# Kernel optimization log

Measured on AMD Instinct MI355X. Metric: run time of the kernel, lower is better.

The kernel has to match this reference:

```python
import jax, jax.numpy as jnp
import numpy as np

B, N, E, D, AD = 8, 1000, 4, 64, 32  # batch, n_node, n_edge_types, state_dim, annotation_dim
W_SCALE = 0.02  # matches normal_(0.0, 0.02) init


def setup_inputs() -> dict:
    key = jax.random.key(0)
    ks = jax.random.split(key, 10)
    return {
        "prop_state": jax.random.normal(ks[0], (B, N, D), jnp.float32),
        "annotation": jax.random.normal(ks[1], (B, N, AD), jnp.float32),
        "A": jax.random.uniform(ks[2], (B, N, 2 * N * E), jnp.float32),
        "W_in": W_SCALE * jax.random.normal(ks[3], (E, D, D), jnp.float32),
        "W_out": W_SCALE * jax.random.normal(ks[4], (E, D, D), jnp.float32),
        "W_r": W_SCALE * jax.random.normal(ks[5], (D, 3 * D), jnp.float32),
        "W_z": W_SCALE * jax.random.normal(ks[6], (D, 3 * D), jnp.float32),
        "W_h": W_SCALE * jax.random.normal(ks[7], (D, 3 * D), jnp.float32),
        "Wo1": W_SCALE * jax.random.normal(ks[8], (D, D + AD), jnp.float32),
        "Wo2": W_SCALE * jax.random.normal(ks[9], (1, D), jnp.float32),
    }


def _propagate(state, A_in, A_out, W_in, W_out, W_r, W_z, W_h):
    b, n, d = state.shape
    e = W_in.shape[0]
    # per-edge-type linear transforms (torch Linear: y = x @ W.T), batched over edge types
    # layout matches torch: stack over e then transpose(0,1) -> [b, e, n, d] -> [b, e*n, d]
    s_in = jnp.einsum('bnd,efd->benf', state, W_in).reshape(b, e * n, d)
    s_out = jnp.einsum('bnd,efd->benf', state, W_out).reshape(b, e * n, d)
    a_in = jnp.matmul(A_in, s_in)    # [b, n, d]
    a_out = jnp.matmul(A_out, s_out)  # [b, n, d]
    a = jnp.concatenate([a_in, a_out, state], axis=2)  # [b, n, 3d]
    r = jax.nn.sigmoid(a @ W_r.T)
    z = jax.nn.sigmoid(a @ W_z.T)
    joined = jnp.concatenate([a_in, a_out, r * state], axis=2)
    h_hat = jnp.tanh(joined @ W_h.T)
    return (1.0 - z) * state + z * h_hat


def reference(prop_state, annotation, A, W_in, W_out, W_r, W_z, W_h, Wo1, Wo2):
    n = prop_state.shape[1]
    e = W_in.shape[0]
    ne = n * e
    A_in, A_out = A[:, :, :ne], A[:, :, ne:]
    # exactly two propagation steps (n_steps_flag path in the original)
    s1 = _propagate(prop_state, A_in, A_out, W_in, W_out, W_r, W_z, W_h)
    s2 = _propagate(s1, A_in, A_out, W_in, W_out, W_r, W_z, W_h)
    join_state = jnp.concatenate([s2, annotation], axis=2)  # [b, n, d+ad]
    out = jnp.tanh(join_state @ Wo1.T) @ Wo2.T  # [b, n, 1]
    return out.sum(axis=2)  # [b, n]
```

## Files before the change

### kernel.cpp

```cpp
#include <hip/hip_runtime.h>


typedef float  f32x4_t  __attribute__((ext_vector_type(4)));
typedef __bf16 bf16x8_t __attribute__((ext_vector_type(8)));
typedef __bf16 bf16x4_t __attribute__((ext_vector_type(4)));

#define MFMA16(a, b, c) __builtin_amdgcn_mfma_f32_16x16x32_bf16((a), (b), (c), 0, 0, 0)

static constexpr int kB  = 8;
static constexpr int kN  = 1000;
static constexpr int kD  = 64;
static constexpr int kAD = 32;
static constexpr int kNE = 4000;
static constexpr int kBN = 8000;
static constexpr int kP  = kBN * kD;

__device__ __forceinline__ float4 ld4(const float* p) {
    return *reinterpret_cast<const float4*>(p);
}

__device__ __forceinline__ float4 ldnt4(const float* p) {
    const f32x4_t v = __builtin_nontemporal_load(reinterpret_cast<const f32x4_t*>(p));
    return make_float4(v.x, v.y, v.z, v.w);
}

__device__ __forceinline__ bf16x8_t cvt8(float4 a, float4 b) {
    bf16x8_t r;
    r[0] = (__bf16)a.x; r[1] = (__bf16)a.y; r[2] = (__bf16)a.z; r[3] = (__bf16)a.w;
    r[4] = (__bf16)b.x; r[5] = (__bf16)b.y; r[6] = (__bf16)b.z; r[7] = (__bf16)b.w;
    return r;
}

__device__ __forceinline__ bf16x8_t sum8(const float* p0, const float* p1) {
    const float4 a0 = ld4(p0), a1 = ld4(p0 + 4);
    const float4 b0 = ld4(p1), b1 = ld4(p1 + 4);
    bf16x8_t r;
    r[0] = (__bf16)(a0.x + b0.x); r[1] = (__bf16)(a0.y + b0.y);
    r[2] = (__bf16)(a0.z + b0.z); r[3] = (__bf16)(a0.w + b0.w);
    r[4] = (__bf16)(a1.x + b1.x); r[5] = (__bf16)(a1.y + b1.y);
    r[6] = (__bf16)(a1.z + b1.z); r[7] = (__bf16)(a1.w + b1.w);
    return r;
}

__device__ __forceinline__ float sigm(float x) {
    x = fminf(fmaxf(x, -30.f), 30.f);
    return 1.0f / (1.0f + __expf(-x));
}

__device__ __forceinline__ float fast_tanh(float x) {
    x = fminf(fmaxf(x, -15.f), 15.f);
    const float e = __expf(-2.0f * x);
    return (1.0f - e) / (1.0f + e);
}

__global__ __launch_bounds__(256) void precompute_swt(
    const float* __restrict__ state,
    const float* __restrict__ W_in,
    const float* __restrict__ W_out,
    __bf16* __restrict__ SWT)
{
    const int bx = blockIdx.x;
    const int jt = bx & 15;
    const int e  = (bx >> 4) & 3;
    const int h  = (bx >> 6) & 1;
    const int b  = bx >> 7;
    const float* W = (h ? W_out : W_in) + e * kD * kD;

    const int tid  = threadIdx.x;
    const int w    = tid >> 6;
    const int lane = tid & 63;
    const int m    = lane & 15;
    const int q    = lane >> 4;

    __shared__ __bf16 T[64][72];

    const int  jj    = jt * 64 + w * 16 + m;
    const bool valid = (jj < kN);
    const float* srow = state + ((size_t)b * kN + (valid ? jj : kN - 1)) * kD + q * 8;
    float4 a0 = ld4(srow),      a1 = ld4(srow + 4);
    float4 a2 = ld4(srow + 32), a3 = ld4(srow + 36);
    if (!valid) {
        a0 = make_float4(0.f, 0.f, 0.f, 0.f); a1 = a0; a2 = a0; a3 = a0;
    }
    const bf16x8_t af0 = cvt8(a0, a1);
    const bf16x8_t af1 = cvt8(a2, a3);

    #pragma unroll
    for (int c = 0; c < 4; ++c) {
        const int f = c * 16 + m;
        const float* wrow = W + f * kD + q * 8;
        const bf16x8_t bf0 = cvt8(ld4(wrow),      ld4(wrow + 4));
        const bf16x8_t bf1 = cvt8(ld4(wrow + 32), ld4(wrow + 36));
        f32x4_t acc = {0.f, 0.f, 0.f, 0.f};
        acc = MFMA16(af0, bf0, acc);
        acc = MFMA16(af1, bf1, acc);
        const int j0 = w * 16 + q * 4;
        bf16x4_t v;
        v[0] = (__bf16)acc[0]; v[1] = (__bf16)acc[1];
        v[2] = (__bf16)acc[2]; v[3] = (__bf16)acc[3];
        *reinterpret_cast<bf16x4_t*>(&T[f][j0]) = v;
    }
    __syncthreads();

    const size_t rowbase = (size_t)((b * 2 + h) * kD);
    #pragma unroll
    for (int rep = 0; rep < 2; ++rep) {
        const int cc = tid + rep * 256;
        const int f  = cc >> 3;
        const int ch = cc & 7;
        const int jj0 = jt * 64 + ch * 8;
        if (jj0 < kN) {
            const uint4 v = *reinterpret_cast<uint4*>(&T[f][ch * 8]);
            *reinterpret_cast<uint4*>(SWT + (rowbase + f) * kNE + e * kN + jj0) = v;
        }
    }
}

__global__ __launch_bounds__(256, 2) void big_mm(
    const float* __restrict__ A,
    const __bf16* __restrict__ SWT,
    float* __restrict__ a_in_p,
    float* __restrict__ a_out_p)
{
    const int bx   = blockIdx.x;
    const int tile = bx & 15;
    const int h    = (bx >> 4) & 1;
    const int b    = (bx >> 5) & 7;
    const int ks   = (bx >> 8) & 1;
    const int tid  = threadIdx.x;
    const int w    = tid >> 6;
    const int lane = tid & 63;
    const int m    = lane & 15;
    const int q    = lane >> 4;

    const int row  = tile * 64 + w * 16 + m;
    const int rowc = row < kN ? row : kN - 1;
    const int kbeg = ks * 1984;

    const float*  Ap = A + ((size_t)b * kN + rowc) * (2 * kNE) + h * kNE + kbeg + q * 8;
    const __bf16* SW = SWT + ((size_t)(b * 2 + h) * kD) * kNE + kbeg + q * 8;
    const __bf16* SB0 = SW + (size_t)(0 * 16 + m) * kNE;
    const __bf16* SB1 = SW + (size_t)(1 * 16 + m) * kNE;
    const __bf16* SB2 = SW + (size_t)(2 * 16 + m) * kNE;
    const __bf16* SB3 = SW + (size_t)(3 * 16 + m) * kNE;

    f32x4_t acc0 = {0.f, 0.f, 0.f, 0.f};
    f32x4_t acc1 = {0.f, 0.f, 0.f, 0.f};
    f32x4_t acc2 = {0.f, 0.f, 0.f, 0.f};
    f32x4_t acc3 = {0.f, 0.f, 0.f, 0.f};

    bf16x8_t ca0 = cvt8(ldnt4(Ap + 0),  ldnt4(Ap + 4));
    bf16x8_t ca1 = cvt8(ldnt4(Ap + 32), ldnt4(Ap + 36));
    bf16x8_t cb00 = *(const bf16x8_t*)(SB0);
    bf16x8_t cb01 = *(const bf16x8_t*)(SB1);
    bf16x8_t cb02 = *(const bf16x8_t*)(SB2);
    bf16x8_t cb03 = *(const bf16x8_t*)(SB3);
    bf16x8_t cb10 = *(const bf16x8_t*)(SB0 + 32);
    bf16x8_t cb11 = *(const bf16x8_t*)(SB1 + 32);
    bf16x8_t cb12 = *(const bf16x8_t*)(SB2 + 32);
    bf16x8_t cb13 = *(const bf16x8_t*)(SB3 + 32);

    for (int kk = 0; kk < 31; ++kk) {
        const int kn = (kk + 1) * 64;
        const int k2 = (kk < 30) ? (kn + 32) : 0;

        const float4 x0 = ldnt4(Ap + kn),  x1 = ldnt4(Ap + kn + 4);
        const float4 x2 = ldnt4(Ap + k2),  x3 = ldnt4(Ap + k2 + 4);
        const bf16x8_t nb00 = *(const bf16x8_t*)(SB0 + kn);
        const bf16x8_t nb01 = *(const bf16x8_t*)(SB1 + kn);
        const bf16x8_t nb02 = *(const bf16x8_t*)(SB2 + kn);
        const bf16x8_t nb03 = *(const bf16x8_t*)(SB3 + kn);
        const bf16x8_t nb10 = *(const bf16x8_t*)(SB0 + k2);
        const bf16x8_t nb11 = *(const bf16x8_t*)(SB1 + k2);
        const bf16x8_t nb12 = *(const bf16x8_t*)(SB2 + k2);
        const bf16x8_t nb13 = *(const bf16x8_t*)(SB3 + k2);

        acc0 = MFMA16(ca0, cb00, acc0);
        acc1 = MFMA16(ca0, cb01, acc1);
        acc2 = MFMA16(ca0, cb02, acc2);
        acc3 = MFMA16(ca0, cb03, acc3);
        acc0 = MFMA16(ca1, cb10, acc0);
        acc1 = MFMA16(ca1, cb11, acc1);
        acc2 = MFMA16(ca1, cb12, acc2);
        acc3 = MFMA16(ca1, cb13, acc3);

        ca0 = cvt8(x0, x1);
        ca1 = cvt8(x2, x3);
        cb00 = nb00; cb01 = nb01; cb02 = nb02; cb03 = nb03;
        cb10 = nb10; cb11 = nb11; cb12 = nb12; cb13 = nb13;
    }
    if (ks == 1) {
        acc0 = MFMA16(ca0, cb00, acc0);
        acc1 = MFMA16(ca0, cb01, acc1);
        acc2 = MFMA16(ca0, cb02, acc2);
        acc3 = MFMA16(ca0, cb03, acc3);
    }

    float* dst = (h ? a_out_p : a_in_p) + (size_t)ks * kP + (size_t)b * kN * kD;
    const int i0 = tile * 64 + w * 16 + q * 4;
    #pragma unroll
    for (int r = 0; r < 4; ++r) {
        const int i = i0 + r;
        if (i < kN) {
            float* drow = dst + (size_t)i * kD + m;
            drow[0]  = acc0[r];
            drow[16] = acc1[r];
            drow[32] = acc2[r];
            drow[48] = acc3[r];
        }
    }
}

__global__ __launch_bounds__(256, 2) void gating(
    const float* __restrict__ a_in_p,
    const float* __restrict__ a_out_p,
    const float* __restrict__ state,
    const float* __restrict__ W_r,
    const float* __restrict__ W_z,
    const float* __restrict__ W_h,
    float* __restrict__ s_next,
    const float* __restrict__ ann,
    const float* __restrict__ Wo1,
    const float* __restrict__ Wo2,
    float* __restrict__ out,
    const int step)
{
    const int i0   = blockIdx.x * 16;
    const int tid  = threadIdx.x;
    const int c    = tid >> 6;
    const int lane = tid & 63;
    const int m    = lane & 15;
    const int q    = lane >> 4;
    const int f    = c * 16 + m;

    __shared__ __bf16 TL[16][72];
    __shared__ float  Osum[4][16];

    const size_t rowA = (size_t)(i0 + m);

    bf16x8_t xf[6];
    {
        const float* p = a_in_p + rowA * kD + q * 8;
        xf[0] = sum8(p,      p + kP);
        xf[1] = sum8(p + 32, p + 32 + kP);
        p = a_out_p + rowA * kD + q * 8;
        xf[2] = sum8(p,      p + kP);
        xf[3] = sum8(p + 32, p + 32 + kP);
        p = state + rowA * kD + q * 8;
        xf[4] = cvt8(ld4(p),      ld4(p + 4));
        xf[5] = cvt8(ld4(p + 32), ld4(p + 36));
    }

    f32x4_t accr = {0.f, 0.f, 0.f, 0.f};
    f32x4_t accz = {0.f, 0.f, 0.f, 0.f};
    f32x4_t acch = {0.f, 0.f, 0.f, 0.f};

    const float* wr = W_r + f * 192 + q * 8;
    const float* wz = W_z + f * 192 + q * 8;
    const float* wh = W_h + f * 192 + q * 8;
    #pragma unroll
    for (int kc = 0; kc < 6; ++kc) {
        accr = MFMA16(xf[kc], cvt8(ld4(wr + kc * 32), ld4(wr + kc * 32 + 4)), accr);
        accz = MFMA16(xf[kc], cvt8(ld4(wz + kc * 32), ld4(wz + kc * 32 + 4)), accz);
        if (kc < 4)
            acch = MFMA16(xf[kc], cvt8(ld4(wh + kc * 32), ld4(wh + kc * 32 + 4)), acch);
    }

    float sC[4];
    #pragma unroll
    for (int r = 0; r < 4; ++r)
        sC[r] = state[(size_t)(i0 + q * 4 + r) * kD + f];

    #pragma unroll
    for (int r = 0; r < 4; ++r)
        TL[q * 4 + r][f] = (__bf16)(sigm(accr[r]) * sC[r]);
    __syncthreads();
    const bf16x8_t rs0 = *(const bf16x8_t*)&TL[m][q * 8];
    const bf16x8_t rs1 = *(const bf16x8_t*)&TL[m][32 + q * 8];

    const float* wh3 = W_h + f * 192 + 128 + q * 8;
    acch = MFMA16(rs0, cvt8(ld4(wh3),      ld4(wh3 + 4)),  acch);
    acch = MFMA16(rs1, cvt8(ld4(wh3 + 32), ld4(wh3 + 36)), acch);

    float ns[4];
    #pragma unroll
    for (int r = 0; r < 4; ++r) {
        const float zv = sigm(accz[r]);
        ns[r] = (1.f - zv) * sC[r] + zv * fast_tanh(acch[r]);
    }

    if (step == 1) {
        #pragma unroll
        for (int r = 0; r < 4; ++r)
            s_next[(size_t)(i0 + q * 4 + r) * kD + f] = ns[r];
    } else {
        __syncthreads();
        #pragma unroll
        for (int r = 0; r < 4; ++r)
            TL[q * 4 + r][f] = (__bf16)ns[r];
        __syncthreads();
        const bf16x8_t j0 = *(const bf16x8_t*)&TL[m][q * 8];
        const bf16x8_t j1 = *(const bf16x8_t*)&TL[m][32 + q * 8];
        const float* ap = ann + rowA * kAD + q * 8;
        const bf16x8_t j2 = cvt8(ld4(ap), ld4(ap + 4));

        f32x4_t acco = {0.f, 0.f, 0.f, 0.f};
        const float* wo = Wo1 + (size_t)f * 96 + q * 8;
        acco = MFMA16(j0, cvt8(ld4(wo),      ld4(wo + 4)),  acco);
        acco = MFMA16(j1, cvt8(ld4(wo + 32), ld4(wo + 36)), acco);
        acco = MFMA16(j2, cvt8(ld4(wo + 64), ld4(wo + 68)), acco);

        const float w2 = Wo2[f];
        float vs[4];
        #pragma unroll
        for (int r = 0; r < 4; ++r)
            vs[r] = fast_tanh(acco[r]) * w2;
        #pragma unroll
        for (int off = 1; off <= 8; off <<= 1) {
            #pragma unroll
            for (int r = 0; r < 4; ++r)
                vs[r] += __shfl_xor(vs[r], off, 64);
        }
        if (m == 0) {
            #pragma unroll
            for (int r = 0; r < 4; ++r)
                Osum[c][q * 4 + r] = vs[r];
        }
        __syncthreads();
        if (tid < 16)
            out[i0 + tid] = Osum[0][tid] + Osum[1][tid] + Osum[2][tid] + Osum[3][tid];
    }
}

extern "C" void kernel_launch(void* const* d_in, const int* in_sizes, int n_in,
                              void* d_out, int out_size, void* d_ws, size_t ws_size,
                              hipStream_t stream) {
    (void)in_sizes; (void)n_in; (void)out_size; (void)ws_size;

    const float* prop_state = (const float*)d_in[0];
    const float* annotation = (const float*)d_in[1];
    const float* A          = (const float*)d_in[2];
    const float* W_in       = (const float*)d_in[3];
    const float* W_out      = (const float*)d_in[4];
    const float* W_r        = (const float*)d_in[5];
    const float* W_z        = (const float*)d_in[6];
    const float* W_h        = (const float*)d_in[7];
    const float* Wo1        = (const float*)d_in[8];
    const float* Wo2        = (const float*)d_in[9];
    float* out = (float*)d_out;

    char* ws = (char*)d_ws;
    __bf16* SWT    = (__bf16*)(ws);
    float*  a_in_p = (float*)(ws + 8192000);
    float*  a_out_p= (float*)(ws + 12288000);
    float*  s1     = (float*)(ws + 16384000);

    precompute_swt<<<1024, 256, 0, stream>>>(prop_state, W_in, W_out, SWT);
    big_mm<<<512, 256, 0, stream>>>(A, SWT, a_in_p, a_out_p);
    gating<<<500, 256, 0, stream>>>(a_in_p, a_out_p, prop_state, W_r, W_z, W_h,
                                    s1, nullptr, nullptr, nullptr, nullptr, 1);
    precompute_swt<<<1024, 256, 0, stream>>>(s1, W_in, W_out, SWT);
    big_mm<<<512, 256, 0, stream>>>(A, SWT, a_in_p, a_out_p);
    gating<<<500, 256, 0, stream>>>(a_in_p, a_out_p, s1, W_r, W_z, W_h,
                                    nullptr, annotation, Wo1, Wo2, out, 2);
}
```

Before: 549.4 us.

## Pre-convert A to bf16 MFMA fragment layout and split K four ways

A new kernel converts A once per call into a bf16 layout ordered like the MFMA fragments. Both propagation GEMMs then read contiguous 16-byte fragments instead of strided fp32 rows that need conversion. SWT is also written in fragment order, and the big GEMM now splits K into four parts across 1024 blocks, with the gating kernel summing four partials. This costs an extra write pass of A and a 128MB workspace, in exchange for halving the bytes each GEMM reads and giving it simpler, more parallel loads.

```diff
diff --git a/kernel.cpp b/kernel.cpp
--- a/kernel.cpp
+++ b/kernel.cpp
@@ -7,21 +7,15 @@
 
 #define MFMA16(a, b, c) __builtin_amdgcn_mfma_f32_16x16x32_bf16((a), (b), (c), 0, 0, 0)
 
-static constexpr int kB  = 8;
-static constexpr int kN  = 1000;
-static constexpr int kD  = 64;
-static constexpr int kAD = 32;
-static constexpr int kNE = 4000;
-static constexpr int kBN = 8000;
-static constexpr int kP  = kBN * kD;
+static constexpr int kN     = 1000;
+static constexpr int kD     = 64;
+static constexpr int kAD    = 32;
+static constexpr int kNE    = 4000;
+static constexpr int kSteps = 125;
+static constexpr int kP     = 8000 * 64;
 
 __device__ __forceinline__ float4 ld4(const float* p) {
     return *reinterpret_cast<const float4*>(p);
-}
-
-__device__ __forceinline__ float4 ldnt4(const float* p) {
-    const f32x4_t v = __builtin_nontemporal_load(reinterpret_cast<const f32x4_t*>(p));
-    return make_float4(v.x, v.y, v.z, v.w);
 }
 
 __device__ __forceinline__ bf16x8_t cvt8(float4 a, float4 b) {
@@ -31,14 +25,19 @@
     return r;
 }
 
-__device__ __forceinline__ bf16x8_t sum8(const float* p0, const float* p1) {
-    const float4 a0 = ld4(p0), a1 = ld4(p0 + 4);
-    const float4 b0 = ld4(p1), b1 = ld4(p1 + 4);
+__device__ __forceinline__ bf16x8_t sum4p(const float* p) {
+    float s0 = 0.f, s1 = 0.f, s2 = 0.f, s3 = 0.f;
+    float s4 = 0.f, s5 = 0.f, s6 = 0.f, s7 = 0.f;
+    #pragma unroll
+    for (int pl = 0; pl < 4; ++pl) {
+        const float4 a0 = ld4(p + (size_t)pl * kP);
+        const float4 a1 = ld4(p + (size_t)pl * kP + 4);
+        s0 += a0.x; s1 += a0.y; s2 += a0.z; s3 += a0.w;
+        s4 += a1.x; s5 += a1.y; s6 += a1.z; s7 += a1.w;
+    }
     bf16x8_t r;
-    r[0] = (__bf16)(a0.x + b0.x); r[1] = (__bf16)(a0.y + b0.y);
-    r[2] = (__bf16)(a0.z + b0.z); r[3] = (__bf16)(a0.w + b0.w);
-    r[4] = (__bf16)(a1.x + b1.x); r[5] = (__bf16)(a1.y + b1.y);
-    r[6] = (__bf16)(a1.z + b1.z); r[7] = (__bf16)(a1.w + b1.w);
+    r[0] = (__bf16)s0; r[1] = (__bf16)s1; r[2] = (__bf16)s2; r[3] = (__bf16)s3;
+    r[4] = (__bf16)s4; r[5] = (__bf16)s5; r[6] = (__bf16)s6; r[7] = (__bf16)s7;
     return r;
 }
 
@@ -53,11 +52,60 @@
     return (1.0f - e) / (1.0f + e);
 }
 
+__global__ __launch_bounds__(256, 4) void relayout_A(
+    const float* __restrict__ A, __bf16* __restrict__ Afrag)
+{
+    const int bx   = blockIdx.x;
+    const int tile = bx & 15;
+    const int rest = bx >> 4;
+    const int kseg = rest % 5;
+    const int rhb  = rest / 5;
+    const int h    = rhb & 1;
+    const int b    = rhb >> 1;
+
+    const int t    = threadIdx.x;
+    const int wv   = t >> 6;
+    const int lane = t & 63;
+    const int m    = lane & 15;
+    const int q    = lane >> 4;
+
+    __shared__ float L[64][133];
+
+    const float* Abase = A + (size_t)b * kN * 8000 + h * 4000;
+    const int sbase = kseg * 25;
+
+    for (int kc = 0; kc < 800; kc += 128) {
+        const int cw  = (kc < 768) ? 128 : 32;
+        const int shl = (kc < 768) ? 5 : 3;
+        const int rounds = (kc < 768) ? 8 : 2;
+        const int kabs = kseg * 800 + kc;
+        for (int p = 0; p < rounds; ++p) {
+            const int idx = p * 256 + t;
+            const int r   = idx >> shl;
+            const int c4  = idx & ((cw >> 2) - 1);
+            int i = tile * 64 + r;
+            if (i >= kN) i = kN - 1;
+            const float4 v = ld4(Abase + (size_t)i * 8000 + kabs + c4 * 4);
+            *reinterpret_cast<float4*>(&L[r][c4 * 4]) = v;
+        }
+        __syncthreads();
+        const int nst = cw >> 5;
+        for (int sp = 0; sp < nst; ++sp) {
+            const float4 a0 = *reinterpret_cast<const float4*>(&L[wv * 16 + m][sp * 32 + q * 8]);
+            const float4 a1 = *reinterpret_cast<const float4*>(&L[wv * 16 + m][sp * 32 + q * 8 + 4]);
+            const int s = sbase + (kc >> 5) + sp;
+            const size_t el = ((((size_t)((b * 2 + h) * 64 + tile * 4 + wv)) * 125 + s) * 64 + lane) * 8;
+            *reinterpret_cast<bf16x8_t*>(Afrag + el) = cvt8(a0, a1);
+        }
+        __syncthreads();
+    }
+}
+
 __global__ __launch_bounds__(256) void precompute_swt(
     const float* __restrict__ state,
     const float* __restrict__ W_in,
     const float* __restrict__ W_out,
-    __bf16* __restrict__ SWT)
+    __bf16* __restrict__ SWTfrag)
 {
     const int bx = blockIdx.x;
     const int jt = bx & 15;
@@ -102,23 +150,27 @@
     }
     __syncthreads();
 
-    const size_t rowbase = (size_t)((b * 2 + h) * kD);
+    const int bh = b * 2 + h;
     #pragma unroll
     for (int rep = 0; rep < 2; ++rep) {
-        const int cc = tid + rep * 256;
-        const int f  = cc >> 3;
-        const int ch = cc & 7;
-        const int jj0 = jt * 64 + ch * 8;
-        if (jj0 < kN) {
-            const uint4 v = *reinterpret_cast<uint4*>(&T[f][ch * 8]);
-            *reinterpret_cast<uint4*>(SWT + (rowbase + f) * kNE + e * kN + jj0) = v;
-        }
-    }
-}
-
-__global__ __launch_bounds__(256, 2) void big_mm(
-    const float* __restrict__ A,
-    const __bf16* __restrict__ SWT,
+        const int m2 = tid & 15;
+        const int cc = (tid >> 4) & 3;
+        const int ol = (tid >> 6) + rep * 4;
+        const int j0 = jt * 64 + ol * 8;
+        if (j0 < kN) {
+            const int jg = e * kN + j0;
+            const int s  = jg >> 5;
+            const int qq = (jg >> 3) & 3;
+            const uint4 v = *reinterpret_cast<uint4*>(&T[cc * 16 + m2][ol * 8]);
+            const size_t el = ((((size_t)bh * 125 + s) * 4 + cc) * 64 + qq * 16 + m2) * 8;
+            *reinterpret_cast<uint4*>((__bf16*)SWTfrag + el) = v;
+        }
+    }
+}
+
+__global__ __launch_bounds__(256, 4) void big_mm_f(
+    const __bf16* __restrict__ Afrag,
+    const __bf16* __restrict__ SWTfrag,
     float* __restrict__ a_in_p,
     float* __restrict__ a_out_p)
 {
@@ -126,78 +178,54 @@
     const int tile = bx & 15;
     const int h    = (bx >> 4) & 1;
     const int b    = (bx >> 5) & 7;
-    const int ks   = (bx >> 8) & 1;
-    const int tid  = threadIdx.x;
-    const int w    = tid >> 6;
-    const int lane = tid & 63;
+    const int ksp  = bx >> 8;
+    const int t    = threadIdx.x;
+    const int wv   = t >> 6;
+    const int lane = t & 63;
     const int m    = lane & 15;
     const int q    = lane >> 4;
 
-    const int row  = tile * 64 + w * 16 + m;
-    const int rowc = row < kN ? row : kN - 1;
-    const int kbeg = ks * 1984;
-
-    const float*  Ap = A + ((size_t)b * kN + rowc) * (2 * kNE) + h * kNE + kbeg + q * 8;
-    const __bf16* SW = SWT + ((size_t)(b * 2 + h) * kD) * kNE + kbeg + q * 8;
-    const __bf16* SB0 = SW + (size_t)(0 * 16 + m) * kNE;
-    const __bf16* SB1 = SW + (size_t)(1 * 16 + m) * kNE;
-    const __bf16* SB2 = SW + (size_t)(2 * 16 + m) * kNE;
-    const __bf16* SB3 = SW + (size_t)(3 * 16 + m) * kNE;
+    const int s0   = ksp * 32;
+    const int send = (s0 + 32 < kSteps) ? s0 + 32 : kSteps;
+    const int ns   = send - s0;
+
+    const int bh = b * 2 + h;
+    const __bf16* pA = Afrag +
+        ((((size_t)(bh * 64 + tile * 4 + wv)) * 125 + s0) * 64 + lane) * 8;
+    const __bf16* pB = SWTfrag +
+        (((size_t)bh * 125 + s0) * 4 * 64) * 8 + (size_t)lane * 8;
 
     f32x4_t acc0 = {0.f, 0.f, 0.f, 0.f};
     f32x4_t acc1 = {0.f, 0.f, 0.f, 0.f};
     f32x4_t acc2 = {0.f, 0.f, 0.f, 0.f};
     f32x4_t acc3 = {0.f, 0.f, 0.f, 0.f};
 
-    bf16x8_t ca0 = cvt8(ldnt4(Ap + 0),  ldnt4(Ap + 4));
-    bf16x8_t ca1 = cvt8(ldnt4(Ap + 32), ldnt4(Ap + 36));
-    bf16x8_t cb00 = *(const bf16x8_t*)(SB0);
-    bf16x8_t cb01 = *(const bf16x8_t*)(SB1);
-    bf16x8_t cb02 = *(const bf16x8_t*)(SB2);
-    bf16x8_t cb03 = *(const bf16x8_t*)(SB3);
-    bf16x8_t cb10 = *(const bf16x8_t*)(SB0 + 32);
-    bf16x8_t cb11 = *(const bf16x8_t*)(SB1 + 32);
-    bf16x8_t cb12 = *(const bf16x8_t*)(SB2 + 32);
-    bf16x8_t cb13 = *(const bf16x8_t*)(SB3 + 32);
-
-    for (int kk = 0; kk < 31; ++kk) {
-        const int kn = (kk + 1) * 64;
-        const int k2 = (kk < 30) ? (kn + 32) : 0;
-
-        const float4 x0 = ldnt4(Ap + kn),  x1 = ldnt4(Ap + kn + 4);
-        const float4 x2 = ldnt4(Ap + k2),  x3 = ldnt4(Ap + k2 + 4);
-        const bf16x8_t nb00 = *(const bf16x8_t*)(SB0 + kn);
-        const bf16x8_t nb01 = *(const bf16x8_t*)(SB1 + kn);
-        const bf16x8_t nb02 = *(const bf16x8_t*)(SB2 + kn);
-        const bf16x8_t nb03 = *(const bf16x8_t*)(SB3 + kn);
-        const bf16x8_t nb10 = *(const bf16x8_t*)(SB0 + k2);
-        const bf16x8_t nb11 = *(const bf16x8_t*)(SB1 + k2);
-        const bf16x8_t nb12 = *(const bf16x8_t*)(SB2 + k2);
-        const bf16x8_t nb13 = *(const bf16x8_t*)(SB3 + k2);
-
-        acc0 = MFMA16(ca0, cb00, acc0);
-        acc1 = MFMA16(ca0, cb01, acc1);
-        acc2 = MFMA16(ca0, cb02, acc2);
-        acc3 = MFMA16(ca0, cb03, acc3);
-        acc0 = MFMA16(ca1, cb10, acc0);
-        acc1 = MFMA16(ca1, cb11, acc1);
-        acc2 = MFMA16(ca1, cb12, acc2);
-        acc3 = MFMA16(ca1, cb13, acc3);
-
-        ca0 = cvt8(x0, x1);
-        ca1 = cvt8(x2, x3);
-        cb00 = nb00; cb01 = nb01; cb02 = nb02; cb03 = nb03;
-        cb10 = nb10; cb11 = nb11; cb12 = nb12; cb13 = nb13;
-    }
-    if (ks == 1) {
-        acc0 = MFMA16(ca0, cb00, acc0);
-        acc1 = MFMA16(ca0, cb01, acc1);
-        acc2 = MFMA16(ca0, cb02, acc2);
-        acc3 = MFMA16(ca0, cb03, acc3);
-    }
-
-    float* dst = (h ? a_out_p : a_in_p) + (size_t)ks * kP + (size_t)b * kN * kD;
-    const int i0 = tile * 64 + w * 16 + q * 4;
+    bf16x8_t cA  = *(const bf16x8_t*)(pA);
+    bf16x8_t cB0 = *(const bf16x8_t*)(pB);
+    bf16x8_t cB1 = *(const bf16x8_t*)(pB + 512);
+    bf16x8_t cB2 = *(const bf16x8_t*)(pB + 1024);
+    bf16x8_t cB3 = *(const bf16x8_t*)(pB + 1536);
+
+    for (int s = 0; s < ns; ++s) {
+        const int adv = (s + 1 < ns) ? 1 : 0;
+        pA += adv * 512;
+        pB += adv * 2048;
+        const bf16x8_t nA  = *(const bf16x8_t*)(pA);
+        const bf16x8_t nB0 = *(const bf16x8_t*)(pB);
+        const bf16x8_t nB1 = *(const bf16x8_t*)(pB + 512);
+        const bf16x8_t nB2 = *(const bf16x8_t*)(pB + 1024);
+        const bf16x8_t nB3 = *(const bf16x8_t*)(pB + 1536);
+
+        acc0 = MFMA16(cA, cB0, acc0);
+        acc1 = MFMA16(cA, cB1, acc1);
+        acc2 = MFMA16(cA, cB2, acc2);
+        acc3 = MFMA16(cA, cB3, acc3);
+
+        cA = nA; cB0 = nB0; cB1 = nB1; cB2 = nB2; cB3 = nB3;
+    }
+
+    float* dst = (h ? a_out_p : a_in_p) + (size_t)ksp * kP + (size_t)b * kN * kD;
+    const int i0 = tile * 64 + wv * 16 + q * 4;
     #pragma unroll
     for (int r = 0; r < 4; ++r) {
         const int i = i0 + r;
@@ -241,11 +269,11 @@
     bf16x8_t xf[6];
     {
         const float* p = a_in_p + rowA * kD + q * 8;
-        xf[0] = sum8(p,      p + kP);
-        xf[1] = sum8(p + 32, p + 32 + kP);
+        xf[0] = sum4p(p);
+        xf[1] = sum4p(p + 32);
         p = a_out_p + rowA * kD + q * 8;
-        xf[2] = sum8(p,      p + kP);
-        xf[3] = sum8(p + 32, p + 32 + kP);
+        xf[2] = sum4p(p);
+        xf[3] = sum4p(p + 32);
         p = state + rowA * kD + q * 8;
         xf[4] = cvt8(ld4(p),      ld4(p + 4));
         xf[5] = cvt8(ld4(p + 32), ld4(p + 36));
@@ -350,17 +378,20 @@
     float* out = (float*)d_out;
 
     char* ws = (char*)d_ws;
-    __bf16* SWT    = (__bf16*)(ws);
-    float*  a_in_p = (float*)(ws + 8192000);
-    float*  a_out_p= (float*)(ws + 12288000);
-    float*  s1     = (float*)(ws + 16384000);
-
-    precompute_swt<<<1024, 256, 0, stream>>>(prop_state, W_in, W_out, SWT);
-    big_mm<<<512, 256, 0, stream>>>(A, SWT, a_in_p, a_out_p);
+    __bf16* Afrag   = (__bf16*)(ws);
+    __bf16* SWTfrag = (__bf16*)(ws + 131072000);
+    float*  a_in_p  = (float*)(ws + 139264000);
+    float*  a_out_p = (float*)(ws + 147456000);
+    float*  s1      = (float*)(ws + 155648000);
+
+    relayout_A<<<1280, 256, 0, stream>>>(A, Afrag);
+
+    precompute_swt<<<1024, 256, 0, stream>>>(prop_state, W_in, W_out, SWTfrag);
+    big_mm_f<<<1024, 256, 0, stream>>>(Afrag, SWTfrag, a_in_p, a_out_p);
     gating<<<500, 256, 0, stream>>>(a_in_p, a_out_p, prop_state, W_r, W_z, W_h,
                                     s1, nullptr, nullptr, nullptr, nullptr, 1);
-    precompute_swt<<<1024, 256, 0, stream>>>(s1, W_in, W_out, SWT);
-    big_mm<<<512, 256, 0, stream>>>(A, SWT, a_in_p, a_out_p);
+    precompute_swt<<<1024, 256, 0, stream>>>(s1, W_in, W_out, SWTfrag);
+    big_mm_f<<<1024, 256, 0, stream>>>(Afrag, SWTfrag, a_in_p, a_out_p);
     gating<<<500, 256, 0, stream>>>(a_in_p, a_out_p, s1, W_r, W_z, W_h,
                                     nullptr, annotation, Wo1, Wo2, out, 2);
 }
```

Result: faster. 514.9 us (-6.3%).
